# Kernel tuning notes

Hardware: AMD Instinct MI355X
Metric: run time of the kernel (lower is better)

## Reference

```python
import jax, jax.numpy as jnp
import numpy as np

K_SIZE = 5  # local window
PAD = K_SIZE // 2


def setup_inputs() -> dict:
    key = jax.random.key(0)
    k1, k2, k3, k4 = jax.random.split(key, 4)
    B, H, W, C = 8, 128, 128, 64
    heads, d = 4, 16  # intermediate_dim=64 split over 4 heads
    return {
        "main": jax.random.normal(k1, (B, H, W, C), dtype=jnp.float32),
        "ref": jax.random.normal(k2, (B, H, W, C), dtype=jnp.float32),
        "W_main": jax.random.normal(k3, (heads, C, d), dtype=jnp.float32) * (2.0 / C) ** 0.5,
        "W_ref": jax.random.normal(k4, (heads, C, d), dtype=jnp.float32) * (2.0 / C) ** 0.5,
    }


def reference(main, ref, W_main, W_ref):
    # 1x1 conv projections per head: [n, B, H, W, d]
    q = jnp.einsum('bhwc,ncd->nbhwd', main, W_main)
    k = jnp.einsum('bhwc,ncd->nbhwd', ref, W_ref)
    B, H, W = main.shape[0], main.shape[1], main.shape[2]
    # SAME zero padding as tf.image.extract_patches
    kp = jnp.pad(k, ((0, 0), (0, 0), (PAD, PAD), (PAD, PAD), (0, 0)))
    # Score against each of the k_size*k_size shifted neighbors (row-major di, dj
    # matching extract_patches + Reshape ordering), without materializing patches.
    scores = [
        jnp.sum(q * kp[:, :, di:di + H, dj:dj + W, :], axis=-1)
        for di in range(K_SIZE) for dj in range(K_SIZE)
    ]
    # Extra key: the (projected) main pixel itself, concatenated last.
    scores.append(jnp.sum(q * q, axis=-1))
    attn = jax.nn.softmax(jnp.stack(scores, axis=-1), axis=-1)  # [n,B,H,W,k*k+1]
    # aggregation_mode == 'average' over heads
    return jnp.mean(attn, axis=0)  # [B,H,W,k*k+1]
```

## Files before the change

### kernel.cpp

```cpp
#include <hip/hip_runtime.h>

#define Bn 8
#define Hn 128
#define Wn 128
#define Cn 64
#define Dn 16
#define NS 26
#define NPX (Bn * Hn * Wn)

#define KPW 132
#define KP_IMG (KPW * KPW)
#define NBORD 66560

#define WS_Q_OFF_B   16384
#define WS_KP_OFF_B  (WS_Q_OFF_B + 8 * NPX * 16)
#define WS_NEEDED    ((size_t)WS_KP_OFF_B + (size_t)64 * KP_IMG * 16)

typedef _Float16 h2    __attribute__((ext_vector_type(2)));
typedef _Float16 f16x8 __attribute__((ext_vector_type(8)));
typedef float    f32x4 __attribute__((ext_vector_type(4)));

__device__ __forceinline__ unsigned int pkf16(float a, float b) {
    return __builtin_bit_cast(unsigned int, __builtin_amdgcn_cvt_pkrtz(a, b));
}
__device__ __forceinline__ float f16lo(unsigned int u) {
    return (float)__builtin_bit_cast(_Float16, (unsigned short)(u & 0xffffu));
}
__device__ __forceinline__ float f16hi(unsigned int u) {
    return (float)__builtin_bit_cast(_Float16, (unsigned short)(u >> 16));
}
__device__ __forceinline__ float dot2(unsigned int a, unsigned int b, float c) {
    return __builtin_amdgcn_fdot2(__builtin_bit_cast(h2, a),
                                  __builtin_bit_cast(h2, b), c, false);
}
__device__ __forceinline__ f16x8 pk8(float4 a, float4 b) {
    const uint4 u = make_uint4(pkf16(a.x, a.y), pkf16(a.z, a.w),
                               pkf16(b.x, b.y), pkf16(b.z, b.w));
    return __builtin_bit_cast(f16x8, u);
}

__global__ __launch_bounds__(256, 2)
void proj_k(const float* __restrict__ refp,
            const float* __restrict__ Wr,
            const float* __restrict__ Wm,
            uint2* __restrict__ kp2,
            uint4* __restrict__ kp4,
            uint4* __restrict__ wfm)
{
    __shared__ uint4 sW[512];

    const int tid = threadIdx.x;
    const int wg  = blockIdx.x;
    const int sw  = ((wg & 7) << 6) | (wg >> 3);

    {
        const int idx = wg * 256 + tid;
        if (idx < 512) {
            const int h  = idx >> 7;
            const int kt = (idx >> 6) & 1;
            const int l  = idx & 63;
            const int dd = l & 15;
            const int cb = kt * 32 + ((l >> 4) << 3);
            const float* base = Wm + h * (Cn * Dn) + dd;
            uint4 v;
            v.x = pkf16(base[(cb + 0) * Dn], base[(cb + 1) * Dn]);
            v.y = pkf16(base[(cb + 2) * Dn], base[(cb + 3) * Dn]);
            v.z = pkf16(base[(cb + 4) * Dn], base[(cb + 5) * Dn]);
            v.w = pkf16(base[(cb + 6) * Dn], base[(cb + 7) * Dn]);
            wfm[idx] = v;
        }
    }

    {
        if (tid < 130) {
            const int idx = wg * 130 + tid;
            const int pb = idx / 1040;
            const int r  = idx - pb * 1040;
            int row, col;
            if (r < 528) { const int q = r / 132; row = (q < 2) ? q : 128 + q; col = r - q * 132; }
            else { const int r2 = r - 528; const int s = r2 & 3; row = 2 + (r2 >> 2); col = (s < 2) ? s : 128 + s; }
            kp4[(size_t)pb * KP_IMG + row * KPW + col] = make_uint4(0, 0, 0, 0);
        }
    }

    for (int e = tid; e < 512; e += 256) {
        const int h  = e >> 7;
        const int kt = (e >> 6) & 1;
        const int l  = e & 63;
        const int dd = l & 15;
        const int cb = kt * 32 + ((l >> 4) << 3);
        const float* base = Wr + h * (Cn * Dn) + dd;
        uint4 v;
        v.x = pkf16(base[(cb + 0) * Dn], base[(cb + 1) * Dn]);
        v.y = pkf16(base[(cb + 2) * Dn], base[(cb + 3) * Dn]);
        v.z = pkf16(base[(cb + 4) * Dn], base[(cb + 5) * Dn]);
        v.w = pkf16(base[(cb + 6) * Dn], base[(cb + 7) * Dn]);
        sW[e] = v;
    }

    const int lane = tid & 63;
    const int wv   = tid >> 6;
    const int px16 = lane & 15;
    const int lg   = lane >> 4;
    const int wbase = sw * 256 + wv * 64;

    float4 raw[16];
#pragma unroll
    for (int g = 0; g < 4; ++g) {
        const float* rrow = refp + (size_t)(wbase + g * 16 + px16) * Cn + lg * 8;
        raw[g * 4 + 0] = *(const float4*)(rrow);
        raw[g * 4 + 1] = *(const float4*)(rrow + 4);
        raw[g * 4 + 2] = *(const float4*)(rrow + 32);
        raw[g * 4 + 3] = *(const float4*)(rrow + 36);
    }

    __syncthreads();

    f16x8 br[4][2];
#pragma unroll
    for (int h = 0; h < 4; ++h)
#pragma unroll
        for (int t = 0; t < 2; ++t)
            br[h][t] = __builtin_bit_cast(f16x8, sW[(h * 2 + t) * 64 + lane]);

    const int halfsel  = lg >> 1;
    const int wordpair = lg & 1;

#pragma unroll
    for (int g = 0; g < 4; ++g) {
        const f16x8 Ar0 = pk8(raw[g * 4 + 0], raw[g * 4 + 1]);
        const f16x8 Ar1 = pk8(raw[g * 4 + 2], raw[g * 4 + 3]);
        const int px = wbase + g * 16 + px16;
        const int bb = px >> 14;
        const int yy = (px & 16383) >> 7;
        const int xx = px & 127;
        const int o  = (yy + 2) * KPW + (xx + 2);
#pragma unroll
        for (int h = 0; h < 4; ++h) {
            f32x4 z = {0.f, 0.f, 0.f, 0.f};
            z = __builtin_amdgcn_mfma_f32_16x16x32_f16(br[h][0], Ar0, z, 0, 0, 0);
            z = __builtin_amdgcn_mfma_f32_16x16x32_f16(br[h][1], Ar1, z, 0, 0, 0);
            const int w = h * 2 + halfsel;
            kp2[((size_t)(w * 8 + bb) * KP_IMG + o) * 2 + wordpair] =
                make_uint2(pkf16(z[0], z[1]), pkf16(z[2], z[3]));
        }
    }
}

__global__ __launch_bounds__(256, 4)
void attn_row_fq(const float* __restrict__ mainp,
                 const uint4* __restrict__ wfm,
                 const uint4* __restrict__ kp,
                 float* __restrict__ out)
{
    __shared__ __align__(16) unsigned int sU[3328];

    const int tid  = threadIdx.x;
    const int lane = tid & 63;
    const int wv   = tid >> 6;
    const int wg = blockIdx.x;
    const int sw = ((wg & 7) << 8) | (wg >> 3);
    const int b  = sw >> 8;
    const int y  = (sw >> 1) & 127;
    const int x0 = (sw & 1) * 64;

    const int px16 = lane & 15;
    const int lg   = lane >> 4;
    const float* mrow = mainp +
        (size_t)((b * Hn + y) * Wn + x0 + wv * 16 + px16) * Cn + lg * 8;
    const float4 m0 = *(const float4*)(mrow);
    const float4 m1 = *(const float4*)(mrow + 4);
    const float4 m2 = *(const float4*)(mrow + 32);
    const float4 m3 = *(const float4*)(mrow + 36);

    f16x8 bm[4][2];
#pragma unroll
    for (int h = 0; h < 4; ++h)
#pragma unroll
        for (int t = 0; t < 2; ++t)
            bm[h][t] = __builtin_bit_cast(f16x8, wfm[(h * 2 + t) * 64 + lane]);

    const f16x8 Am0 = pk8(m0, m1), Am1 = pk8(m2, m3);
#pragma unroll
    for (int h = 0; h < 4; ++h) {
        f32x4 z = {0.f, 0.f, 0.f, 0.f};
        z = __builtin_amdgcn_mfma_f32_16x16x32_f16(bm[h][0], Am0, z, 0, 0, 0);
        z = __builtin_amdgcn_mfma_f32_16x16x32_f16(bm[h][1], Am1, z, 0, 0, 0);
        *(uint2*)&sU[(h * 64 + wv * 16 + px16) * 8 + lg * 2] =
            make_uint2(pkf16(z[0], z[1]), pkf16(z[2], z[3]));
    }

    __syncthreads();

    const int head = __builtin_amdgcn_readfirstlane(wv);
    const uint4 qa = *(const uint4*)&sU[(head * 64 + lane) * 8];
    const uint4 qb = *(const uint4*)&sU[(head * 64 + lane) * 8 + 4];

    const uint4* klo = kp + ((head * 2 + 0) * 8 + b) * KP_IMG;
    const uint4* khi = kp + ((head * 2 + 1) * 8 + b) * KP_IMG;

    float sc[NS];
#pragma unroll
    for (int di = 0; di < 5; ++di) {
        const int p0 = (y + di) * KPW + x0 + lane;
        uint4 kl[5], kh[5];
#pragma unroll
        for (int dj = 0; dj < 5; ++dj) { kl[dj] = klo[p0 + dj]; kh[dj] = khi[p0 + dj]; }
#pragma unroll
        for (int dj = 0; dj < 5; ++dj) {
            float s0 = dot2(qa.x, kl[dj].x, 0.f);
            float s1 = dot2(qb.x, kh[dj].x, 0.f);
            s0 = dot2(qa.y, kl[dj].y, s0);
            s1 = dot2(qb.y, kh[dj].y, s1);
            s0 = dot2(qa.z, kl[dj].z, s0);
            s1 = dot2(qb.z, kh[dj].z, s1);
            s0 = dot2(qa.w, kl[dj].w, s0);
            s1 = dot2(qb.w, kh[dj].w, s1);
            sc[di * 5 + dj] = s0 + s1;
        }
    }
    {
        float s0 = dot2(qa.x, qa.x, 0.f);
        float s1 = dot2(qb.x, qb.x, 0.f);
        s0 = dot2(qa.y, qa.y, s0);
        s1 = dot2(qb.y, qb.y, s1);
        s0 = dot2(qa.z, qa.z, s0);
        s1 = dot2(qb.z, qb.z, s1);
        s0 = dot2(qa.w, qa.w, s0);
        s1 = dot2(qb.w, qb.w, s1);
        sc[25] = s0 + s1;
    }

    float mx = sc[0];
#pragma unroll
    for (int i = 1; i < NS; ++i) mx = fmaxf(mx, sc[i]);
    float ssum = 0.f;
#pragma unroll
    for (int i = 0; i < NS; ++i) { sc[i] = __expf(sc[i] - mx); ssum += sc[i]; }
    const float inv = 1.0f / ssum;
#pragma unroll
    for (int i = 0; i < NS; ++i) sc[i] *= inv;

    __syncthreads();

    {
        unsigned int* myrow = sU + (wv * 64 + lane) * 13;
#pragma unroll
        for (int j = 0; j < 13; ++j) myrow[j] = pkf16(sc[2 * j], sc[2 * j + 1]);
    }
    __syncthreads();

    const size_t ob = ((size_t)(b * Hn + y) * Wn + x0) * NS;
    for (int idx = tid; idx < 64 * 13; idx += 256) {
        const int px = idx / 13;
        const int p  = idx - px * 13;
        const unsigned int u0 = sU[(0 * 64 + px) * 13 + p];
        const unsigned int u1 = sU[(1 * 64 + px) * 13 + p];
        const unsigned int u2 = sU[(2 * 64 + px) * 13 + p];
        const unsigned int u3 = sU[(3 * 64 + px) * 13 + p];
        const float lo = f16lo(u0) + f16lo(u1) + f16lo(u2) + f16lo(u3);
        const float hi = f16hi(u0) + f16hi(u1) + f16hi(u2) + f16hi(u3);
        *(float2*)(out + ob + (size_t)px * NS + 2 * p) =
            make_float2(lo * 0.25f, hi * 0.25f);
    }
}

#define TILE 8
#define HALO 12
#define NHALO (HALO * HALO)
#define PXW 36
__global__ void pack_weights(const float* __restrict__ Wm,
                             const float* __restrict__ Wr,
                             unsigned int* __restrict__ wp) {
    const int idx = blockIdx.x * 256 + threadIdx.x;
    if (idx < 2 * 4 * 32 * Dn) {
        const int t = idx >> 11;
        const int r = idx & 2047;
        const int h = r >> 9;
        const int m = (r >> 4) & 31;
        const int d = r & 15;
        const float* W = t ? Wr : Wm;
        wp[idx] = pkf16(W[h * (Cn * Dn) + (2 * m) * Dn + d],
                        W[h * (Cn * Dn) + (2 * m + 1) * Dn + d]);
    }
}
__global__ __launch_bounds__(256, 4)
void local_attn_fused_r4(const float* __restrict__ mainp,
                         const float* __restrict__ refp,
                         const unsigned int* __restrict__ wp,
                         float* __restrict__ out)
{
    __shared__ unsigned int sK[NHALO * PXW];
    const int tid  = threadIdx.x;
    const int lane = tid & 63;
    const int wv   = tid >> 6;
    const int head = __builtin_amdgcn_readfirstlane(wv);
    const int b    = blockIdx.z;
    const int y0   = blockIdx.y * TILE;
    const int x0   = blockIdx.x * TILE;
    const unsigned int* wmh = wp + head * (32 * Dn);
    const unsigned int* wrh = wp + 2048 + head * (32 * Dn);
    for (int p = lane; p < NHALO; p += 64) {
        const int hr = p / HALO;
        const int hc = p - hr * HALO;
        const int gy = y0 - 2 + hr;
        const int gx = x0 - 2 + hc;
        float acc[Dn];
#pragma unroll
        for (int d = 0; d < Dn; ++d) acc[d] = 0.f;
        if ((unsigned)gy < (unsigned)Hn && (unsigned)gx < (unsigned)Wn) {
            const float4* rp4 = (const float4*)(refp + (((size_t)b * Hn + gy) * Wn + gx) * Cn);
#pragma unroll
            for (int c4 = 0; c4 < Cn / 4; ++c4) {
                const float4 rv = rp4[c4];
                const unsigned int r01 = pkf16(rv.x, rv.y);
                const unsigned int r23 = pkf16(rv.z, rv.w);
                const unsigned int* w0 = wrh + (2 * c4) * Dn;
                const unsigned int* w1 = wrh + (2 * c4 + 1) * Dn;
#pragma unroll
                for (int d = 0; d < Dn; ++d) acc[d] = dot2(r01, w0[d], acc[d]);
#pragma unroll
                for (int d = 0; d < Dn; ++d) acc[d] = dot2(r23, w1[d], acc[d]);
            }
        }
        unsigned int pk[8];
#pragma unroll
        for (int j = 0; j < 8; ++j) pk[j] = pkf16(acc[2 * j], acc[2 * j + 1]);
        unsigned int* dst = sK + p * PXW + head * 8;
        *(uint4*)(dst)     = make_uint4(pk[0], pk[1], pk[2], pk[3]);
        *(uint4*)(dst + 4) = make_uint4(pk[4], pk[5], pk[6], pk[7]);
    }
    const int pr = lane >> 3;
    const int pc = lane & 7;
    const float4* mp4 = (const float4*)(mainp + (((size_t)b * Hn + (y0 + pr)) * Wn + (x0 + pc)) * Cn);
    float q[Dn];
#pragma unroll
    for (int d = 0; d < Dn; ++d) q[d] = 0.f;
#pragma unroll
    for (int c4 = 0; c4 < Cn / 4; ++c4) {
        const float4 mv = mp4[c4];
        const unsigned int m01 = pkf16(mv.x, mv.y);
        const unsigned int m23 = pkf16(mv.z, mv.w);
        const unsigned int* w0 = wmh + (2 * c4) * Dn;
        const unsigned int* w1 = wmh + (2 * c4 + 1) * Dn;
#pragma unroll
        for (int d = 0; d < Dn; ++d) q[d] = dot2(m01, w0[d], q[d]);
#pragma unroll
        for (int d = 0; d < Dn; ++d) q[d] = dot2(m23, w1[d], q[d]);
    }
    unsigned int qh[8];
#pragma unroll
    for (int j = 0; j < 8; ++j) qh[j] = pkf16(q[2 * j], q[2 * j + 1]);
    __syncthreads();
    float sc[NS];
#pragma unroll
    for (int di = 0; di < 5; ++di) {
#pragma unroll
        for (int dj = 0; dj < 5; ++dj) {
            const int h = (pr + di) * HALO + (pc + dj);
            const unsigned int* src = sK + h * PXW + head * 8;
            const uint4 ka = *(const uint4*)(src);
            const uint4 kb = *(const uint4*)(src + 4);
            float s;
            s = dot2(qh[0], ka.x, 0.f);
            s = dot2(qh[1], ka.y, s);
            s = dot2(qh[2], ka.z, s);
            s = dot2(qh[3], ka.w, s);
            s = dot2(qh[4], kb.x, s);
            s = dot2(qh[5], kb.y, s);
            s = dot2(qh[6], kb.z, s);
            s = dot2(qh[7], kb.w, s);
            sc[di * 5 + dj] = s;
        }
    }
    {
        float s = q[0] * q[0];
#pragma unroll
        for (int d = 1; d < Dn; ++d) s = fmaf(q[d], q[d], s);
        sc[25] = s;
    }
    float mx = sc[0];
#pragma unroll
    for (int i = 1; i < NS; ++i) mx = fmaxf(mx, sc[i]);
    float ssum = 0.f;
#pragma unroll
    for (int i = 0; i < NS; ++i) { sc[i] = __expf(sc[i] - mx); ssum += sc[i]; }
    const float inv = 1.0f / ssum;
#pragma unroll
    for (int i = 0; i < NS; ++i) sc[i] *= inv;
    __syncthreads();
    {
        unsigned int* myrow = sK + (wv * 64 + lane) * 14;
#pragma unroll
        for (int j = 0; j < 13; ++j) myrow[j] = pkf16(sc[2 * j], sc[2 * j + 1]);
    }
    __syncthreads();
    const unsigned short* sA = (const unsigned short*)sK;
    const size_t obase = (((size_t)b * Hn + y0) * Wn + x0) * NS;
    for (int idx = tid; idx < TILE * TILE * NS; idx += 256) {
        const int r   = idx / (TILE * NS);
        const int t   = idx - r * (TILE * NS);
        const int c   = t / NS;
        const int i   = t - c * NS;
        const int ppx = r * TILE + c;
        float acc = 0.f;
#pragma unroll
        for (int h = 0; h < 4; ++h)
            acc += (float)__builtin_bit_cast(_Float16, sA[(h * 64 + ppx) * 28 + i]);
        out[obase + (size_t)r * (Wn * NS) + t] = 0.25f * acc;
    }
}

extern "C" void kernel_launch(void* const* d_in, const int* in_sizes, int n_in,
                              void* d_out, int out_size, void* d_ws, size_t ws_size,
                              hipStream_t stream) {
    (void)in_sizes; (void)n_in; (void)out_size;
    const float* mainp = (const float*)d_in[0];
    const float* refp  = (const float*)d_in[1];
    const float* Wm    = (const float*)d_in[2];
    const float* Wr    = (const float*)d_in[3];
    float* out = (float*)d_out;

    if (ws_size >= WS_NEEDED) {
        uint4* wfm = (uint4*)d_ws;
        uint4* kpb = (uint4*)((char*)d_ws + WS_KP_OFF_B);
        proj_k<<<512, 256, 0, stream>>>(refp, Wr, Wm, (uint2*)kpb, kpb, wfm);
        attn_row_fq<<<2048, 256, 0, stream>>>(mainp, wfm, kpb, out);
    } else {
        unsigned int* wpk = (unsigned int*)d_ws;
        pack_weights<<<16, 256, 0, stream>>>(Wm, Wr, wpk);
        dim3 grid2(Wn / TILE, Hn / TILE, Bn);
        local_attn_fused_r4<<<grid2, 256, 0, stream>>>(mainp, refp, wpk, out);
    }
}
```

Before: 36.66 us.

## Fuse projection and attention into one cooperative kernel with grid sync

Replaces the two-launch sequence (key projection, then attention) with a single cooperative kernel of 1024 blocks. Each block first projects a slice of ref keys into the padded buffer, prefetches its main rows, then does a grid-wide sync and processes two attention tiles. This removes one launch gap and the drain between kernels and overlaps the main-row loads with the sync. In exchange it adds the cost of a grid barrier, an occupancy query on every launch, and fewer blocks doing more serial work each.

```diff
diff --git a/kernel.cpp b/kernel.cpp
--- a/kernel.cpp
+++ b/kernel.cpp
@@ -1,4 +1,5 @@
 #include <hip/hip_runtime.h>
+#include <hip/hip_cooperative_groups.h>
 
 #define Bn 8
 #define Hn 128
@@ -37,6 +38,214 @@
     const uint4 u = make_uint4(pkf16(a.x, a.y), pkf16(a.z, a.w),
                                pkf16(b.x, b.y), pkf16(b.z, b.w));
     return __builtin_bit_cast(f16x8, u);
+}
+__device__ __forceinline__ void pack_w_entry(const float* W, int e, uint4* dst) {
+    const int h  = e >> 7;
+    const int kt = (e >> 6) & 1;
+    const int l  = e & 63;
+    const int dd = l & 15;
+    const int cb = kt * 32 + ((l >> 4) << 3);
+    const float* base = W + h * (Cn * Dn) + dd;
+    uint4 v;
+    v.x = pkf16(base[(cb + 0) * Dn], base[(cb + 1) * Dn]);
+    v.y = pkf16(base[(cb + 2) * Dn], base[(cb + 3) * Dn]);
+    v.z = pkf16(base[(cb + 4) * Dn], base[(cb + 5) * Dn]);
+    v.w = pkf16(base[(cb + 6) * Dn], base[(cb + 7) * Dn]);
+    *dst = v;
+}
+
+__global__ __launch_bounds__(256, 4)
+void fused_all(const float* __restrict__ mainp, const float* __restrict__ refp,
+               const float* __restrict__ Wm, const float* __restrict__ Wr,
+               uint2* __restrict__ kp2, uint4* __restrict__ kp4,
+               uint4* __restrict__ wfm, float* __restrict__ out)
+{
+    __shared__ __align__(16) unsigned int sU[3328];
+
+    const int tid  = threadIdx.x;
+    const int blk  = blockIdx.x;
+    const int lane = tid & 63;
+    const int wv   = tid >> 6;
+    const int px16 = lane & 15;
+    const int lg   = lane >> 4;
+
+    if (blk < 2) {
+        const int idx = blk * 256 + tid;
+        pack_w_entry(Wm, idx, &wfm[idx]);
+    }
+    if (tid < 65) {
+        const int idx = blk * 65 + tid;
+        const int pb = idx / 1040;
+        const int r  = idx - pb * 1040;
+        int row, col;
+        if (r < 528) { const int q = r / 132; row = (q < 2) ? q : 128 + q; col = r - q * 132; }
+        else { const int r2 = r - 528; const int s = r2 & 3; row = 2 + (r2 >> 2); col = (s < 2) ? s : 128 + s; }
+        kp4[(size_t)pb * KP_IMG + row * KPW + col] = make_uint4(0, 0, 0, 0);
+    }
+    uint4* sW = (uint4*)sU;
+    for (int e = tid; e < 512; e += 256) pack_w_entry(Wr, e, &sW[e]);
+
+    const int sw1   = ((blk & 7) << 7) | (blk >> 3);
+    const int wbase = sw1 * 128 + wv * 32;
+    float4 raw[8];
+#pragma unroll
+    for (int g = 0; g < 2; ++g) {
+        const float* rrow = refp + (size_t)(wbase + g * 16 + px16) * Cn + lg * 8;
+        raw[g * 4 + 0] = *(const float4*)(rrow);
+        raw[g * 4 + 1] = *(const float4*)(rrow + 4);
+        raw[g * 4 + 2] = *(const float4*)(rrow + 32);
+        raw[g * 4 + 3] = *(const float4*)(rrow + 36);
+    }
+    __syncthreads();
+
+    {
+        f16x8 br[4][2];
+#pragma unroll
+        for (int h = 0; h < 4; ++h)
+#pragma unroll
+            for (int t = 0; t < 2; ++t)
+                br[h][t] = __builtin_bit_cast(f16x8, sW[(h * 2 + t) * 64 + lane]);
+        const int halfsel  = lg >> 1;
+        const int wordpair = lg & 1;
+#pragma unroll
+        for (int g = 0; g < 2; ++g) {
+            const f16x8 Ar0 = pk8(raw[g * 4 + 0], raw[g * 4 + 1]);
+            const f16x8 Ar1 = pk8(raw[g * 4 + 2], raw[g * 4 + 3]);
+            const int px = wbase + g * 16 + px16;
+            const int bb = px >> 14;
+            const int yy = (px & 16383) >> 7;
+            const int xx = px & 127;
+            const int o  = (yy + 2) * KPW + (xx + 2);
+#pragma unroll
+            for (int h = 0; h < 4; ++h) {
+                f32x4 z = {0.f, 0.f, 0.f, 0.f};
+                z = __builtin_amdgcn_mfma_f32_16x16x32_f16(br[h][0], Ar0, z, 0, 0, 0);
+                z = __builtin_amdgcn_mfma_f32_16x16x32_f16(br[h][1], Ar1, z, 0, 0, 0);
+                const int w = h * 2 + halfsel;
+                kp2[((size_t)(w * 8 + bb) * KP_IMG + o) * 2 + wordpair] =
+                    make_uint2(pkf16(z[0], z[1]), pkf16(z[2], z[3]));
+            }
+        }
+    }
+
+    const int b     = blk & 7;
+    const int tile0 = b * 256 + (blk >> 3) * 2;
+    float4 m0, m1, m2, m3;
+    {
+        const int y  = (tile0 >> 1) & 127;
+        const int x0 = (tile0 & 1) * 64;
+        const float* mrow = mainp +
+            (size_t)((b * Hn + y) * Wn + x0 + wv * 16 + px16) * Cn + lg * 8;
+        m0 = *(const float4*)(mrow);
+        m1 = *(const float4*)(mrow + 4);
+        m2 = *(const float4*)(mrow + 32);
+        m3 = *(const float4*)(mrow + 36);
+    }
+
+    cooperative_groups::this_grid().sync();
+
+    f16x8 bm[4][2];
+#pragma unroll
+    for (int h = 0; h < 4; ++h)
+#pragma unroll
+        for (int t = 0; t < 2; ++t)
+            bm[h][t] = __builtin_bit_cast(f16x8, wfm[(h * 2 + t) * 64 + lane]);
+
+    const int head = __builtin_amdgcn_readfirstlane(wv);
+
+    for (int t = 0; t < 2; ++t) {
+        const int tile = tile0 + t;
+        const int y  = (tile >> 1) & 127;
+        const int x0 = (tile & 1) * 64;
+        if (t == 1) {
+            __syncthreads();
+            const float* mrow = mainp +
+                (size_t)((b * Hn + y) * Wn + x0 + wv * 16 + px16) * Cn + lg * 8;
+            m0 = *(const float4*)(mrow);
+            m1 = *(const float4*)(mrow + 4);
+            m2 = *(const float4*)(mrow + 32);
+            m3 = *(const float4*)(mrow + 36);
+        }
+        const f16x8 Am0 = pk8(m0, m1), Am1 = pk8(m2, m3);
+#pragma unroll
+        for (int h = 0; h < 4; ++h) {
+            f32x4 z = {0.f, 0.f, 0.f, 0.f};
+            z = __builtin_amdgcn_mfma_f32_16x16x32_f16(bm[h][0], Am0, z, 0, 0, 0);
+            z = __builtin_amdgcn_mfma_f32_16x16x32_f16(bm[h][1], Am1, z, 0, 0, 0);
+            *(uint2*)&sU[(h * 64 + wv * 16 + px16) * 8 + lg * 2] =
+                make_uint2(pkf16(z[0], z[1]), pkf16(z[2], z[3]));
+        }
+        __syncthreads();
+
+        const uint4 qa = *(const uint4*)&sU[(head * 64 + lane) * 8];
+        const uint4 qb = *(const uint4*)&sU[(head * 64 + lane) * 8 + 4];
+        const uint4* klo = kp4 + ((size_t)(head * 2 + 0) * 8 + b) * KP_IMG;
+        const uint4* khi = kp4 + ((size_t)(head * 2 + 1) * 8 + b) * KP_IMG;
+
+        float sc[NS];
+#pragma unroll
+        for (int di = 0; di < 5; ++di) {
+            const int p0 = (y + di) * KPW + x0 + lane;
+            uint4 kl[5], kh[5];
+#pragma unroll
+            for (int dj = 0; dj < 5; ++dj) { kl[dj] = klo[p0 + dj]; kh[dj] = khi[p0 + dj]; }
+#pragma unroll
+            for (int dj = 0; dj < 5; ++dj) {
+                float s0 = dot2(qa.x, kl[dj].x, 0.f);
+                float s1 = dot2(qb.x, kh[dj].x, 0.f);
+                s0 = dot2(qa.y, kl[dj].y, s0);
+                s1 = dot2(qb.y, kh[dj].y, s1);
+                s0 = dot2(qa.z, kl[dj].z, s0);
+                s1 = dot2(qb.z, kh[dj].z, s1);
+                s0 = dot2(qa.w, kl[dj].w, s0);
+                s1 = dot2(qb.w, kh[dj].w, s1);
+                sc[di * 5 + dj] = s0 + s1;
+            }
+        }
+        {
+            float s0 = dot2(qa.x, qa.x, 0.f);
+            float s1 = dot2(qb.x, qb.x, 0.f);
+            s0 = dot2(qa.y, qa.y, s0);
+            s1 = dot2(qb.y, qb.y, s1);
+            s0 = dot2(qa.z, qa.z, s0);
+            s1 = dot2(qb.z, qb.z, s1);
+            s0 = dot2(qa.w, qa.w, s0);
+            s1 = dot2(qb.w, qb.w, s1);
+            sc[25] = s0 + s1;
+        }
+
+        float mx = sc[0];
+#pragma unroll
+        for (int i = 1; i < NS; ++i) mx = fmaxf(mx, sc[i]);
+        float ssum = 0.f;
+#pragma unroll
+        for (int i = 0; i < NS; ++i) { sc[i] = __expf(sc[i] - mx); ssum += sc[i]; }
+        const float inv = 1.0f / ssum;
+#pragma unroll
+        for (int i = 0; i < NS; ++i) sc[i] *= inv;
+
+        __syncthreads();
+        {
+            unsigned int* myrow = sU + (wv * 64 + lane) * 13;
+#pragma unroll
+            for (int j = 0; j < 13; ++j) myrow[j] = pkf16(sc[2 * j], sc[2 * j + 1]);
+        }
+        __syncthreads();
+
+        const size_t ob = ((size_t)(b * Hn + y) * Wn + x0) * NS;
+        for (int idx = tid; idx < 64 * 13; idx += 256) {
+            const int px = idx / 13;
+            const int p  = idx - px * 13;
+            const unsigned int u0 = sU[(0 * 64 + px) * 13 + p];
+            const unsigned int u1 = sU[(1 * 64 + px) * 13 + p];
+            const unsigned int u2 = sU[(2 * 64 + px) * 13 + p];
+            const unsigned int u3 = sU[(3 * 64 + px) * 13 + p];
+            const float lo = f16lo(u0) + f16lo(u1) + f16lo(u2) + f16lo(u3);
+            const float hi = f16hi(u0) + f16hi(u1) + f16hi(u2) + f16hi(u3);
+            *(float2*)(out + ob + (size_t)px * NS + 2 * p) =
+                make_float2(lo * 0.25f, hi * 0.25f);
+        }
+    }
 }
 
 __global__ __launch_bounds__(256, 2)
@@ -48,62 +257,29 @@
             uint4* __restrict__ wfm)
 {
     __shared__ uint4 sW[512];
-
     const int tid = threadIdx.x;
     const int wg  = blockIdx.x;
     const int sw  = ((wg & 7) << 6) | (wg >> 3);
-
     {
         const int idx = wg * 256 + tid;
-        if (idx < 512) {
-            const int h  = idx >> 7;
-            const int kt = (idx >> 6) & 1;
-            const int l  = idx & 63;
-            const int dd = l & 15;
-            const int cb = kt * 32 + ((l >> 4) << 3);
-            const float* base = Wm + h * (Cn * Dn) + dd;
-            uint4 v;
-            v.x = pkf16(base[(cb + 0) * Dn], base[(cb + 1) * Dn]);
-            v.y = pkf16(base[(cb + 2) * Dn], base[(cb + 3) * Dn]);
-            v.z = pkf16(base[(cb + 4) * Dn], base[(cb + 5) * Dn]);
-            v.w = pkf16(base[(cb + 6) * Dn], base[(cb + 7) * Dn]);
-            wfm[idx] = v;
-        }
-    }
-
-    {
-        if (tid < 130) {
-            const int idx = wg * 130 + tid;
-            const int pb = idx / 1040;
-            const int r  = idx - pb * 1040;
-            int row, col;
-            if (r < 528) { const int q = r / 132; row = (q < 2) ? q : 128 + q; col = r - q * 132; }
-            else { const int r2 = r - 528; const int s = r2 & 3; row = 2 + (r2 >> 2); col = (s < 2) ? s : 128 + s; }
-            kp4[(size_t)pb * KP_IMG + row * KPW + col] = make_uint4(0, 0, 0, 0);
-        }
-    }
-
-    for (int e = tid; e < 512; e += 256) {
-        const int h  = e >> 7;
-        const int kt = (e >> 6) & 1;
-        const int l  = e & 63;
-        const int dd = l & 15;
-        const int cb = kt * 32 + ((l >> 4) << 3);
-        const float* base = Wr + h * (Cn * Dn) + dd;
-        uint4 v;
-        v.x = pkf16(base[(cb + 0) * Dn], base[(cb + 1) * Dn]);
-        v.y = pkf16(base[(cb + 2) * Dn], base[(cb + 3) * Dn]);
-        v.z = pkf16(base[(cb + 4) * Dn], base[(cb + 5) * Dn]);
-        v.w = pkf16(base[(cb + 6) * Dn], base[(cb + 7) * Dn]);
-        sW[e] = v;
-    }
+        if (idx < 512) pack_w_entry(Wm, idx, &wfm[idx]);
+    }
+    if (tid < 130) {
+        const int idx = wg * 130 + tid;
+        const int pb = idx / 1040;
+        const int r  = idx - pb * 1040;
+        int row, col;
+        if (r < 528) { const int q = r / 132; row = (q < 2) ? q : 128 + q; col = r - q * 132; }
+        else { const int r2 = r - 528; const int s = r2 & 3; row = 2 + (r2 >> 2); col = (s < 2) ? s : 128 + s; }
+        kp4[(size_t)pb * KP_IMG + row * KPW + col] = make_uint4(0, 0, 0, 0);
+    }
+    for (int e = tid; e < 512; e += 256) pack_w_entry(Wr, e, &sW[e]);
 
     const int lane = tid & 63;
     const int wv   = tid >> 6;
     const int px16 = lane & 15;
     const int lg   = lane >> 4;
     const int wbase = sw * 256 + wv * 64;
-
     float4 raw[16];
 #pragma unroll
     for (int g = 0; g < 4; ++g) {
@@ -113,19 +289,15 @@
         raw[g * 4 + 2] = *(const float4*)(rrow + 32);
         raw[g * 4 + 3] = *(const float4*)(rrow + 36);
     }
-
-    __syncthreads();
-
+    __syncthreads();
     f16x8 br[4][2];
 #pragma unroll
     for (int h = 0; h < 4; ++h)
 #pragma unroll
         for (int t = 0; t < 2; ++t)
             br[h][t] = __builtin_bit_cast(f16x8, sW[(h * 2 + t) * 64 + lane]);
-
     const int halfsel  = lg >> 1;
     const int wordpair = lg & 1;
-
 #pragma unroll
     for (int g = 0; g < 4; ++g) {
         const f16x8 Ar0 = pk8(raw[g * 4 + 0], raw[g * 4 + 1]);
@@ -154,7 +326,6 @@
                  float* __restrict__ out)
 {
     __shared__ __align__(16) unsigned int sU[3328];
-
     const int tid  = threadIdx.x;
     const int lane = tid & 63;
     const int wv   = tid >> 6;
@@ -163,7 +334,6 @@
     const int b  = sw >> 8;
     const int y  = (sw >> 1) & 127;
     const int x0 = (sw & 1) * 64;
-
     const int px16 = lane & 15;
     const int lg   = lane >> 4;
     const float* mrow = mainp +
@@ -172,14 +342,12 @@
     const float4 m1 = *(const float4*)(mrow + 4);
     const float4 m2 = *(const float4*)(mrow + 32);
     const float4 m3 = *(const float4*)(mrow + 36);
-
     f16x8 bm[4][2];
 #pragma unroll
     for (int h = 0; h < 4; ++h)
 #pragma unroll
         for (int t = 0; t < 2; ++t)
             bm[h][t] = __builtin_bit_cast(f16x8, wfm[(h * 2 + t) * 64 + lane]);
-
     const f16x8 Am0 = pk8(m0, m1), Am1 = pk8(m2, m3);
 #pragma unroll
     for (int h = 0; h < 4; ++h) {
@@ -189,16 +357,12 @@
         *(uint2*)&sU[(h * 64 + wv * 16 + px16) * 8 + lg * 2] =
             make_uint2(pkf16(z[0], z[1]), pkf16(z[2], z[3]));
     }
-
-    __syncthreads();
-
+    __syncthreads();
     const int head = __builtin_amdgcn_readfirstlane(wv);
     const uint4 qa = *(const uint4*)&sU[(head * 64 + lane) * 8];
     const uint4 qb = *(const uint4*)&sU[(head * 64 + lane) * 8 + 4];
-
     const uint4* klo = kp + ((head * 2 + 0) * 8 + b) * KP_IMG;
     const uint4* khi = kp + ((head * 2 + 1) * 8 + b) * KP_IMG;
-
     float sc[NS];
 #pragma unroll
     for (int di = 0; di < 5; ++di) {
@@ -230,7 +394,6 @@
         s1 = dot2(qb.w, qb.w, s1);
         sc[25] = s0 + s1;
     }
-
     float mx = sc[0];
 #pragma unroll
     for (int i = 1; i < NS; ++i) mx = fmaxf(mx, sc[i]);
@@ -240,16 +403,13 @@
     const float inv = 1.0f / ssum;
 #pragma unroll
     for (int i = 0; i < NS; ++i) sc[i] *= inv;
-
-    __syncthreads();
-
+    __syncthreads();
     {
         unsigned int* myrow = sU + (wv * 64 + lane) * 13;
 #pragma unroll
         for (int j = 0; j < 13; ++j) myrow[j] = pkf16(sc[2 * j], sc[2 * j + 1]);
     }
     __syncthreads();
-
     const size_t ob = ((size_t)(b * Hn + y) * Wn + x0) * NS;
     for (int idx = tid; idx < 64 * 13; idx += 256) {
         const int px = idx / 13;
@@ -424,8 +584,19 @@
     if (ws_size >= WS_NEEDED) {
         uint4* wfm = (uint4*)d_ws;
         uint4* kpb = (uint4*)((char*)d_ws + WS_KP_OFF_B);
-        proj_k<<<512, 256, 0, stream>>>(refp, Wr, Wm, (uint2*)kpb, kpb, wfm);
-        attn_row_fq<<<2048, 256, 0, stream>>>(mainp, wfm, kpb, out);
+        uint2* kp2 = (uint2*)kpb;
+
+        int maxb = 0;
+        (void)hipOccupancyMaxActiveBlocksPerMultiprocessor(&maxb, fused_all, 256, 0);
+        if (maxb >= 4) {
+            void* args[] = {(void*)&mainp, (void*)&refp, (void*)&Wm, (void*)&Wr,
+                            (void*)&kp2, (void*)&kpb, (void*)&wfm, (void*)&out};
+            hipLaunchCooperativeKernel((const void*)fused_all, dim3(1024), dim3(256),
+                                       args, 0, stream);
+        } else {
+            proj_k<<<512, 256, 0, stream>>>(refp, Wr, Wm, kp2, kpb, wfm);
+            attn_row_fq<<<2048, 256, 0, stream>>>(mainp, wfm, kpb, out);
+        }
     } else {
         unsigned int* wpk = (unsigned int*)d_ws;
         pack_weights<<<16, 256, 0, stream>>>(Wm, Wr, wpk);
```

Result: no change. 36.91 us (+0.7%).
